# Performance work log

Measured on AMD Instinct MI355X. Metric: run time of the kernel, lower is better.

Reference implementation:

```python
import jax, jax.numpy as jnp
import numpy as np
import math

N_CLASSES = 1000
CODE_LENGTH = 1024
IN_FEATURES = 4096
BATCH = 512
MAX_PROB = 0.95
POWER = 1.0


def _hadamard(n):
    # Sylvester construction; n must be a power of 2.
    H = np.array([[1.0]], dtype=np.float64)
    while H.shape[0] < n:
        H = np.block([[H, H], [H, -H]])
    return H


def setup_inputs() -> dict:
    key = jax.random.key(0)
    k1, k2, k3 = jax.random.split(key, 3)
    x = jax.random.normal(k1, (BATCH, IN_FEATURES), dtype=jnp.float32)
    out_feat = CODE_LENGTH - 1  # single head: code_length//1 - 1
    # nn.Linear default init: U(-1/sqrt(fan_in), 1/sqrt(fan_in))
    bound = 1.0 / math.sqrt(IN_FEATURES)
    W = jax.random.uniform(k2, (out_feat, IN_FEATURES), dtype=jnp.float32, minval=-bound, maxval=bound)
    b = jax.random.uniform(k3, (out_feat,), dtype=jnp.float32, minval=-bound, maxval=bound)
    labels = jnp.asarray(_hadamard(CODE_LENGTH)[:N_CLASSES, 1:], dtype=jnp.float32)  # (C, L-1)
    eps = jnp.float32(CODE_LENGTH * math.pow((1.0 - MAX_PROB) / (MAX_PROB * (N_CLASSES - 1)), 1.0 / POWER))
    power = jnp.float32(POWER)
    return {"x": x, "W": W, "b": b, "labels": labels, "eps": eps, "power": power}


def reference(x, W, b, labels, eps, power):
    # Linear head: (B, in) @ (in, L-1) + b
    h = jnp.tanh(x @ W.T + b)                               # (B, L-1)
    # L1 distance to each Hadamard code row: (B, 1, L-1) vs (C, L-1)
    d = jnp.sum(jnp.abs(h[:, None, :] - labels), axis=-1)   # (B, C)
    d = jnp.maximum(d, eps)
    inv = 1.0 / jnp.power(d, power)                          # (B, C)
    return inv / jnp.sum(inv, axis=-1, keepdims=True)
```

## Files before the change

### kernel.cpp

```cpp
#include <hip/hip_runtime.h>

#define BATCH 512
#define INFEAT 4096
#define LOUT 1023
#define NCLS 1000
#define NPAD 1024
#define SPLITK 8

typedef __bf16 bf16x8 __attribute__((ext_vector_type(8)));
typedef float f32x4 __attribute__((ext_vector_type(4)));

__device__ __forceinline__ unsigned short f2bf(float a) {
    unsigned u = __builtin_bit_cast(unsigned, a);
    return (unsigned short)((u + 0x7fffu + ((u >> 16) & 1u)) >> 16);
}
__device__ __forceinline__ float bf2f(unsigned short u) {
    return __builtin_bit_cast(float, ((unsigned)u) << 16);
}
__device__ __forceinline__ uint4 pack8(float4 a, float4 b) {
    union { __bf16 h[8]; uint4 u; } r;
    r.h[0] = (__bf16)a.x; r.h[1] = (__bf16)a.y;
    r.h[2] = (__bf16)a.z; r.h[3] = (__bf16)a.w;
    r.h[4] = (__bf16)b.x; r.h[5] = (__bf16)b.y;
    r.h[6] = (__bf16)b.z; r.h[7] = (__bf16)b.w;
    return r.u;
}

__global__ __launch_bounds__(512, 1) void k_gemm(
    const float* __restrict__ x, const float* __restrict__ W,
    unsigned short* __restrict__ partial) {
    __shared__ unsigned char lds[65536];
    const int bid = blockIdx.x;
    const int work = (bid & 7) * 32 + (bid >> 3);
    const int bn = work & 7, bm = (work >> 3) & 3, sp = work >> 5;
    const int tid = threadIdx.x;
    const int wave = tid >> 6, lane = tid & 63;
    const int lrow = lane & 15, lgrp = lane >> 4;
    const int wr = wave >> 2, wc = wave & 3;
    const int arow0 = bm * 128, brow0 = bn * 128, chunk0 = sp * 8;

    const int row0 = tid >> 3, jb0 = tid & 7;
    const int row1 = (512 + tid) >> 3, jb1 = tid & 7;

    f32x4 acc[4][2] = {};
    float4 sAa[4], sAb[4], sBa[4], sBb[4];

    auto LOADR = [&](int t, float4 (&aa)[4], float4 (&bb)[4]) {
        const size_t c0 = (size_t)(chunk0 + t) * 64;
        {
            const float4* q = (const float4*)(x + (size_t)(arow0 + row0) * INFEAT + c0 + jb0 * 8);
            aa[0] = q[0]; aa[1] = q[1];
        }
        {
            const float4* q = (const float4*)(x + (size_t)(arow0 + row1) * INFEAT + c0 + jb1 * 8);
            aa[2] = q[0]; aa[3] = q[1];
        }
        {
            int wrow = brow0 + row0;
            if (wrow < LOUT) {
                const float4* q = (const float4*)(W + (size_t)wrow * INFEAT + c0 + jb0 * 8);
                bb[0] = q[0]; bb[1] = q[1];
            } else {
                bb[0] = make_float4(0.f, 0.f, 0.f, 0.f);
                bb[1] = make_float4(0.f, 0.f, 0.f, 0.f);
            }
        }
        {
            int wrow = brow0 + row1;
            if (wrow < LOUT) {
                const float4* q = (const float4*)(W + (size_t)wrow * INFEAT + c0 + jb1 * 8);
                bb[2] = q[0]; bb[3] = q[1];
            } else {
                bb[2] = make_float4(0.f, 0.f, 0.f, 0.f);
                bb[3] = make_float4(0.f, 0.f, 0.f, 0.f);
            }
        }
    };

    auto WRITE = [&](int bsel, float4 (&aa)[4], float4 (&bb)[4]) {
        unsigned char* lA = lds + bsel * 32768;
        unsigned char* lB = lA + 16384;
        *(uint4*)(lA + row0 * 128 + ((jb0 ^ (row0 & 7)) * 16)) = pack8(aa[0], aa[1]);
        *(uint4*)(lA + row1 * 128 + ((jb1 ^ (row1 & 7)) * 16)) = pack8(aa[2], aa[3]);
        *(uint4*)(lB + row0 * 128 + ((jb0 ^ (row0 & 7)) * 16)) = pack8(bb[0], bb[1]);
        *(uint4*)(lB + row1 * 128 + ((jb1 ^ (row1 & 7)) * 16)) = pack8(bb[2], bb[3]);
    };

    auto STEP_BODY = [&](int bsel, float4 (&aa)[4], float4 (&bb)[4],
                         bool do_write, bool do_load, int tload) {
        const unsigned char* lA = lds + bsel * 32768;
        const unsigned char* lB = lA + 16384;
        bf16x8 fa[2][4], fb[2][2];
#pragma unroll
        for (int ks = 0; ks < 2; ++ks) {
            int swz = ((ks * 4 + lgrp) ^ (lrow & 7)) * 16;
#pragma unroll
            for (int m = 0; m < 4; ++m)
                fa[ks][m] = *(const bf16x8*)(lA + (wr * 64 + m * 16 + lrow) * 128 + swz);
#pragma unroll
            for (int n = 0; n < 2; ++n)
                fb[ks][n] = *(const bf16x8*)(lB + (wc * 32 + n * 16 + lrow) * 128 + swz);
        }
        if (do_write) WRITE(bsel ^ 1, aa, bb);
        if (do_load) LOADR(tload, aa, bb);
        __builtin_amdgcn_s_setprio(1);
#pragma unroll
        for (int ks = 0; ks < 2; ++ks)
#pragma unroll
            for (int m = 0; m < 4; ++m)
#pragma unroll
                for (int n = 0; n < 2; ++n)
                    acc[m][n] = __builtin_amdgcn_mfma_f32_16x16x32_bf16(
                        fa[ks][m], fb[ks][n], acc[m][n], 0, 0, 0);
        __builtin_amdgcn_s_setprio(0);
        asm volatile("s_waitcnt lgkmcnt(0)" ::: "memory");
        __builtin_amdgcn_s_barrier();
    };

    LOADR(0, sAa, sAb);
    LOADR(1, sBa, sBb);
    WRITE(0, sAa, sAb);
    LOADR(2, sAa, sAb);
    asm volatile("s_waitcnt lgkmcnt(0)" ::: "memory");
    __builtin_amdgcn_s_barrier();

    STEP_BODY(0, sBa, sBb, true, true, 3);
    STEP_BODY(1, sAa, sAb, true, true, 4);
    STEP_BODY(0, sBa, sBb, true, true, 5);
    STEP_BODY(1, sAa, sAb, true, true, 6);
    STEP_BODY(0, sBa, sBb, true, true, 7);
    STEP_BODY(1, sAa, sAb, true, false, 0);
    STEP_BODY(0, sBa, sBb, true, false, 0);
    STEP_BODY(1, sAa, sAb, false, false, 0);

    unsigned short* P = partial + (size_t)sp * (BATCH * NPAD);
#pragma unroll
    for (int m = 0; m < 4; ++m)
#pragma unroll
        for (int n = 0; n < 2; ++n)
#pragma unroll
            for (int reg = 0; reg < 4; ++reg) {
                int r = arow0 + wr * 64 + m * 16 + lgrp * 4 + reg;
                int c = brow0 + wc * 32 + n * 16 + lrow;
                P[(size_t)r * NPAD + c] = f2bf(acc[m][n][reg]);
            }
}

__global__ __launch_bounds__(256) void k_fused(const unsigned short* __restrict__ partial,
                                               const float* __restrict__ bias,
                                               const float* __restrict__ epsp,
                                               const float* __restrict__ powp,
                                               float* __restrict__ out) {
    __shared__ float g[1024];
    __shared__ float wsum[4];
    const int r = blockIdx.x, t = threadIdx.x;
    const int n0 = t * 4;

    f32x4 v = {0.0f, 0.0f, 0.0f, 0.0f};
#pragma unroll
    for (int s = 0; s < SPLITK; ++s) {
        ushort4 p = *(const ushort4*)(partial + ((size_t)s * BATCH + r) * NPAD + n0);
        v[0] += bf2f(p.x); v[1] += bf2f(p.y); v[2] += bf2f(p.z); v[3] += bf2f(p.w);
    }
    float bb[4];
    if (t < 255) {
        float4 b4 = *(const float4*)(bias + n0);
        bb[0] = b4.x; bb[1] = b4.y; bb[2] = b4.z; bb[3] = b4.w;
    } else {
        bb[0] = bias[1020]; bb[1] = bias[1021]; bb[2] = bias[1022]; bb[3] = 0.0f;
    }
    if (t == 0) g[0] = 0.0f;
#pragma unroll
    for (int j = 0; j < 4; ++j) {
        int n = n0 + j;
        if (n < LOUT) g[n + 1] = tanhf(v[j] + bb[j]);
    }
    __syncthreads();

#pragma unroll 1
    for (int s = 0; s < 10; ++s) {
        int st = 1 << s;
#pragma unroll
        for (int pp = 0; pp < 2; ++pp) {
            int p = t + pp * 256;
            int idx = ((p >> s) << (s + 1)) | (p & (st - 1));
            float a = g[idx], c = g[idx + st];
            g[idx] = a + c;
            g[idx + st] = a - c;
        }
        __syncthreads();
    }

    const float eps = *epsp, pw = *powp;
    float iv[4];
    float ss = 0.0f;
#pragma unroll
    for (int j = 0; j < 4; ++j) {
        int c = n0 + j;
        float d = fmaxf(1023.0f - g[c], eps);
        float q = (pw == 1.0f) ? (1.0f / d) : powf(d, -pw);
        if (c >= NCLS) q = 0.0f;
        iv[j] = q;
        ss += q;
    }
#pragma unroll
    for (int m = 32; m; m >>= 1) ss += __shfl_xor(ss, m, 64);
    if ((t & 63) == 0) wsum[t >> 6] = ss;
    __syncthreads();
    float sc = 1.0f / (wsum[0] + wsum[1] + wsum[2] + wsum[3]);

    if (n0 < NCLS) {
        float4 o;
        o.x = iv[0] * sc; o.y = iv[1] * sc; o.z = iv[2] * sc; o.w = iv[3] * sc;
        *(float4*)(out + (size_t)r * NCLS + n0) = o;
    }
}

extern "C" void kernel_launch(void* const* d_in, const int* in_sizes, int n_in,
                              void* d_out, int out_size, void* d_ws, size_t ws_size,
                              hipStream_t stream) {
    const float* x = (const float*)d_in[0];
    const float* W = (const float*)d_in[1];
    const float* b = (const float*)d_in[2];
    const float* epsp = (const float*)d_in[4];
    const float* powp = (const float*)d_in[5];
    float* out = (float*)d_out;

    unsigned char* ws = (unsigned char*)d_ws;
    unsigned short* partial = (unsigned short*)ws;

    k_gemm<<<256, 512, 0, stream>>>(x, W, partial);
    k_fused<<<512, 256, 0, stream>>>(partial, b, epsp, powp, out);
}
```

Baseline: 26.15 us.

## Shrink GEMM tiles to 64x64 with 256 threads and four blocks per CU

```diff
diff --git a/kernel.cpp b/kernel.cpp
--- a/kernel.cpp
+++ b/kernel.cpp
@@ -26,121 +26,113 @@
     return r.u;
 }
 
-__global__ __launch_bounds__(512, 1) void k_gemm(
+__global__ __launch_bounds__(256, 4) void k_gemm(
     const float* __restrict__ x, const float* __restrict__ W,
     unsigned short* __restrict__ partial) {
-    __shared__ unsigned char lds[65536];
+    __shared__ unsigned char lds[32768];
     const int bid = blockIdx.x;
-    const int work = (bid & 7) * 32 + (bid >> 3);
-    const int bn = work & 7, bm = (work >> 3) & 3, sp = work >> 5;
+    const int work = (bid & 7) * 128 + (bid >> 3);
+    const int bn = work & 15, bm = (work >> 4) & 7, sp = work >> 7;
     const int tid = threadIdx.x;
     const int wave = tid >> 6, lane = tid & 63;
     const int lrow = lane & 15, lgrp = lane >> 4;
-    const int wr = wave >> 2, wc = wave & 3;
-    const int arow0 = bm * 128, brow0 = bn * 128, chunk0 = sp * 8;
+    const int wr = wave >> 1, wc = wave & 1;
+    const int arow0 = bm * 64, brow0 = bn * 64, chunk0 = sp * 8;
 
     const int row0 = tid >> 3, jb0 = tid & 7;
-    const int row1 = (512 + tid) >> 3, jb1 = tid & 7;
-
-    f32x4 acc[4][2] = {};
-    float4 sAa[4], sAb[4], sBa[4], sBb[4];
-
-    auto LOADR = [&](int t, float4 (&aa)[4], float4 (&bb)[4]) {
+    const int row1 = 32 + (tid >> 3), jb1 = tid & 7;
+
+    f32x4 acc[2][2] = {};
+    float4 sa[4], sb[4];
+
+    auto LOADR = [&](int t) {
         const size_t c0 = (size_t)(chunk0 + t) * 64;
         {
             const float4* q = (const float4*)(x + (size_t)(arow0 + row0) * INFEAT + c0 + jb0 * 8);
-            aa[0] = q[0]; aa[1] = q[1];
+            sa[0] = q[0]; sa[1] = q[1];
         }
         {
             const float4* q = (const float4*)(x + (size_t)(arow0 + row1) * INFEAT + c0 + jb1 * 8);
-            aa[2] = q[0]; aa[3] = q[1];
+            sa[2] = q[0]; sa[3] = q[1];
         }
         {
             int wrow = brow0 + row0;
             if (wrow < LOUT) {
                 const float4* q = (const float4*)(W + (size_t)wrow * INFEAT + c0 + jb0 * 8);
-                bb[0] = q[0]; bb[1] = q[1];
+                sb[0] = q[0]; sb[1] = q[1];
             } else {
-                bb[0] = make_float4(0.f, 0.f, 0.f, 0.f);
-                bb[1] = make_float4(0.f, 0.f, 0.f, 0.f);
+                sb[0] = make_float4(0.f, 0.f, 0.f, 0.f);
+                sb[1] = make_float4(0.f, 0.f, 0.f, 0.f);
             }
         }
         {
             int wrow = brow0 + row1;
             if (wrow < LOUT) {
                 const float4* q = (const float4*)(W + (size_t)wrow * INFEAT + c0 + jb1 * 8);
-                bb[2] = q[0]; bb[3] = q[1];
+                sb[2] = q[0]; sb[3] = q[1];
             } else {
-                bb[2] = make_float4(0.f, 0.f, 0.f, 0.f);
-                bb[3] = make_float4(0.f, 0.f, 0.f, 0.f);
+                sb[2] = make_float4(0.f, 0.f, 0.f, 0.f);
+                sb[3] = make_float4(0.f, 0.f, 0.f, 0.f);
             }
         }
     };
 
-    auto WRITE = [&](int bsel, float4 (&aa)[4], float4 (&bb)[4]) {
-        unsigned char* lA = lds + bsel * 32768;
-        unsigned char* lB = lA + 16384;
-        *(uint4*)(lA + row0 * 128 + ((jb0 ^ (row0 & 7)) * 16)) = pack8(aa[0], aa[1]);
-        *(uint4*)(lA + row1 * 128 + ((jb1 ^ (row1 & 7)) * 16)) = pack8(aa[2], aa[3]);
-        *(uint4*)(lB + row0 * 128 + ((jb0 ^ (row0 & 7)) * 16)) = pack8(bb[0], bb[1]);
-        *(uint4*)(lB + row1 * 128 + ((jb1 ^ (row1 & 7)) * 16)) = pack8(bb[2], bb[3]);
+    auto WRITE = [&](int bsel) {
+        unsigned char* lA = lds + bsel * 16384;
+        unsigned char* lB = lA + 8192;
+        *(uint4*)(lA + row0 * 128 + ((jb0 ^ (row0 & 7)) * 16)) = pack8(sa[0], sa[1]);
+        *(uint4*)(lA + row1 * 128 + ((jb1 ^ (row1 & 7)) * 16)) = pack8(sa[2], sa[3]);
+        *(uint4*)(lB + row0 * 128 + ((jb0 ^ (row0 & 7)) * 16)) = pack8(sb[0], sb[1]);
+        *(uint4*)(lB + row1 * 128 + ((jb1 ^ (row1 & 7)) * 16)) = pack8(sb[2], sb[3]);
     };
 
-    auto STEP_BODY = [&](int bsel, float4 (&aa)[4], float4 (&bb)[4],
-                         bool do_write, bool do_load, int tload) {
-        const unsigned char* lA = lds + bsel * 32768;
-        const unsigned char* lB = lA + 16384;
-        bf16x8 fa[2][4], fb[2][2];
+    LOADR(0);
+    WRITE(0);
+    LOADR(1);
+    __syncthreads();
+
+#pragma unroll 1
+    for (int t = 0; t < 8; ++t) {
+        const int cur = t & 1;
+        const unsigned char* lA = lds + cur * 16384;
+        const unsigned char* lB = lA + 8192;
+        bf16x8 fa[2][2], fb[2][2];
 #pragma unroll
         for (int ks = 0; ks < 2; ++ks) {
             int swz = ((ks * 4 + lgrp) ^ (lrow & 7)) * 16;
 #pragma unroll
-            for (int m = 0; m < 4; ++m)
-                fa[ks][m] = *(const bf16x8*)(lA + (wr * 64 + m * 16 + lrow) * 128 + swz);
+            for (int m = 0; m < 2; ++m)
+                fa[ks][m] = *(const bf16x8*)(lA + (wr * 32 + m * 16 + lrow) * 128 + swz);
 #pragma unroll
             for (int n = 0; n < 2; ++n)
                 fb[ks][n] = *(const bf16x8*)(lB + (wc * 32 + n * 16 + lrow) * 128 + swz);
         }
-        if (do_write) WRITE(bsel ^ 1, aa, bb);
-        if (do_load) LOADR(tload, aa, bb);
         __builtin_amdgcn_s_setprio(1);
 #pragma unroll
         for (int ks = 0; ks < 2; ++ks)
 #pragma unroll
-            for (int m = 0; m < 4; ++m)
+            for (int m = 0; m < 2; ++m)
 #pragma unroll
                 for (int n = 0; n < 2; ++n)
                     acc[m][n] = __builtin_amdgcn_mfma_f32_16x16x32_bf16(
                         fa[ks][m], fb[ks][n], acc[m][n], 0, 0, 0);
         __builtin_amdgcn_s_setprio(0);
+        if (t + 1 < 8) {
+            WRITE(cur ^ 1);
+            if (t + 2 < 8) LOADR(t + 2);
+        }
         asm volatile("s_waitcnt lgkmcnt(0)" ::: "memory");
         __builtin_amdgcn_s_barrier();
-    };
-
-    LOADR(0, sAa, sAb);
-    LOADR(1, sBa, sBb);
-    WRITE(0, sAa, sAb);
-    LOADR(2, sAa, sAb);
-    asm volatile("s_waitcnt lgkmcnt(0)" ::: "memory");
-    __builtin_amdgcn_s_barrier();
-
-    STEP_BODY(0, sBa, sBb, true, true, 3);
-    STEP_BODY(1, sAa, sAb, true, true, 4);
-    STEP_BODY(0, sBa, sBb, true, true, 5);
-    STEP_BODY(1, sAa, sAb, true, true, 6);
-    STEP_BODY(0, sBa, sBb, true, true, 7);
-    STEP_BODY(1, sAa, sAb, true, false, 0);
-    STEP_BODY(0, sBa, sBb, true, false, 0);
-    STEP_BODY(1, sAa, sAb, false, false, 0);
+    }
 
     unsigned short* P = partial + (size_t)sp * (BATCH * NPAD);
 #pragma unroll
-    for (int m = 0; m < 4; ++m)
+    for (int m = 0; m < 2; ++m)
 #pragma unroll
         for (int n = 0; n < 2; ++n)
 #pragma unroll
             for (int reg = 0; reg < 4; ++reg) {
-                int r = arow0 + wr * 64 + m * 16 + lgrp * 4 + reg;
+                int r = arow0 + wr * 32 + m * 16 + lgrp * 4 + reg;
                 int c = brow0 + wc * 32 + n * 16 + lrow;
                 P[(size_t)r * NPAD + c] = f2bf(acc[m][n][reg]);
             }
@@ -229,6 +221,6 @@
     unsigned char* ws = (unsigned char*)d_ws;
     unsigned short* partial = (unsigned short*)ws;
 
-    k_gemm<<<256, 512, 0, stream>>>(x, W, partial);
+    k_gemm<<<1024, 256, 0, stream>>>(x, W, partial);
     k_fused<<<512, 256, 0, stream>>>(partial, b, epsp, powp, out);
 }
```

New measurement: 26.34 us. No clear change (+0.7%).
